# Optimization experiments

Measured on AMD Instinct MI355X. Metric: run time of the kernel, lower is better.

Reference implementation:

```python
import jax, jax.numpy as jnp
import numpy as np

NUM_EXPERTS = 8
TOP_K = 2
N_EMBD = 1024
D_FFN = 2048  # 4*N_EMBD // TOP_K, already multiple of BLOCK_N=128
BLOCK_M = 128
NORM_TOPK = True


def setup_inputs() -> dict:
    key = jax.random.key(0)
    k1, k2, k3 = jax.random.split(key, 3)
    x = jax.random.normal(k1, (2, 2048, N_EMBD), dtype=jnp.float32)
    router_w = jax.random.normal(k2, (NUM_EXPERTS, N_EMBD), dtype=jnp.float32) * 0.02
    w1 = jax.random.normal(k3, (N_EMBD, D_FFN * NUM_EXPERTS), dtype=jnp.float32) * 0.02
    return {"x": x, "router_w": router_w, "w1": w1}


def reference(x, router_w, w1):
    B, S, H = x.shape
    x_flat = x.reshape(-1, H)                                   # [T, H]
    router_logits = x_flat @ router_w.T                         # [T, E]
    probs = jax.nn.softmax(router_logits.astype(jnp.float32), axis=-1)
    rweights, sel = jax.lax.top_k(probs, TOP_K)                 # [T, k]
    if NORM_TOPK:
        rweights = rweights / rweights.sum(axis=-1, keepdims=True)
    rweights = rweights.astype(x.dtype)

    # repeat_interleave tokens top_k times, then stable-sort by expert id
    x_rep = jnp.repeat(x_flat, TOP_K, axis=0)                   # [M, H]
    sel_rep = sel.reshape(-1)                                   # [M]
    rw_rep = rweights.reshape(-1, 1)                            # [M, 1]
    order = jnp.argsort(sel_rep, stable=True)                   # expert-sort permutation
    x_grouped = x_rep[order]                                    # [M, H]
    sel_sorted = sel_rep[order]                                 # [M]
    rw_sorted = rw_rep[order]                                   # [M, 1]

    M = x_grouped.shape[0]
    nblk = M // BLOCK_M                                         # M divisible by BLOCK_M by construction
    # SDD kernel: expert of the first row of each BLOCK_M block selects w1 slice
    block_expert = sel_sorted[::BLOCK_M]                        # [nblk] == col_indices_ptr
    w1e = w1.reshape(H, NUM_EXPERTS, D_FFN)                     # w1[:, e*D:(e+1)*D] == w1e[:, e, :]
    w_blk = jnp.take(w1e, block_expert, axis=1)                 # [H, nblk, D]
    x_blk = x_grouped.reshape(nblk, BLOCK_M, H)                 # [nblk, Bm, H]
    block_sparse = jnp.einsum('bmh,hbd->bmd', x_blk, w_blk).reshape(M, D_FFN)

    block_sparse = jax.nn.gelu(block_sparse, approximate=False) * rw_sorted
    return block_sparse, router_logits
```

## Files before the change

### kernel.cpp

```cpp
#include <hip/hip_runtime.h>
#include <hip/hip_bf16.h>
#include <cmath>

typedef float f32x16 __attribute__((ext_vector_type(16)));
typedef __bf16 bf16x8 __attribute__((ext_vector_type(8)));
typedef __bf16 bf16x4 __attribute__((ext_vector_type(4)));

#define NE 8
#define H 1024
#define DF 2048
#define WCOLS 16384
#define NTOK 4096
#define MROWS 8192
#define NBLK 64


typedef const __attribute__((address_space(1))) unsigned int glb_u32;
typedef __attribute__((address_space(3))) unsigned int lds_u32;

__device__ __forceinline__ void async_load16(const void* g, void* l) {
    __builtin_amdgcn_global_load_lds((glb_u32*)g, (lds_u32*)l, 16, 0, 0);
}

__global__ __launch_bounds__(256) void prep_kernel(
    const float* __restrict__ x, const float* __restrict__ rw,
    const float* __restrict__ w1,
    float* __restrict__ logits, int* __restrict__ sel, float* __restrict__ rwn,
    __bf16* __restrict__ xb, __bf16* __restrict__ Wt)
{
    __shared__ float tile[32][132];
    int b = blockIdx.x;
    int tid = threadIdx.x;
    if (b < 1024) {
        int tok  = b * 4 + (tid >> 6);
        int lane = tid & 63;
        const float* xr = x + (size_t)tok * H;
        __bf16* xbr = xb + (size_t)tok * H;
        float acc[NE];
#pragma unroll
        for (int e = 0; e < NE; ++e) acc[e] = 0.f;
#pragma unroll
        for (int it = 0; it < 4; ++it) {
            int k = (it * 64 + lane) * 4;
            float4 xv = *(const float4*)(xr + k);
            bf16x4 xc;
            xc[0] = (__bf16)xv.x; xc[1] = (__bf16)xv.y;
            xc[2] = (__bf16)xv.z; xc[3] = (__bf16)xv.w;
            *(bf16x4*)(xbr + k) = xc;
#pragma unroll
            for (int e = 0; e < NE; ++e) {
                float4 wv = *(const float4*)(rw + e * H + k);
                acc[e] += xv.x * wv.x + xv.y * wv.y + xv.z * wv.z + xv.w * wv.w;
            }
        }
#pragma unroll
        for (int e = 0; e < NE; ++e) {
            float v = acc[e];
#pragma unroll
            for (int off = 32; off > 0; off >>= 1) v += __shfl_xor(v, off, 64);
            acc[e] = v;
        }
        if (lane == 0) {
#pragma unroll
            for (int e = 0; e < NE; ++e) logits[tok * NE + e] = acc[e];
            int i1 = 0; float m1 = acc[0];
#pragma unroll
            for (int e = 1; e < NE; ++e) if (acc[e] > m1) { m1 = acc[e]; i1 = e; }
            int i2 = -1; float m2 = -INFINITY;
#pragma unroll
            for (int e = 0; e < NE; ++e) if (e != i1 && acc[e] > m2) { m2 = acc[e]; i2 = e; }
            float e2 = expf(m2 - m1);
            float inv = 1.f / (1.f + e2);
            sel[tok * 2]     = i1;  sel[tok * 2 + 1] = i2;
            rwn[tok * 2]     = inv; rwn[tok * 2 + 1] = e2 * inv;
        }
        return;
    }
    int g  = b - 1024;
    int c  = g >> 5;
    int kb = g & 31;
    int kk = tid >> 3;
    int cc = (tid & 7) * 16;
    const float* src = w1 + (size_t)(kb * 32 + kk) * WCOLS + c * 128 + cc;
#pragma unroll
    for (int i = 0; i < 4; ++i) {
        float4 v = *(const float4*)(src + i * 4);
        *(float4*)&tile[kk][cc + i * 4] = v;
    }
    __syncthreads();
    int n = tid >> 1, kc0 = (tid & 1) * 16;
    bf16x8 o0, o1;
#pragma unroll
    for (int i = 0; i < 8; ++i) {
        o0[i] = (__bf16)tile[kc0 + i][n];
        o1[i] = (__bf16)tile[kc0 + 8 + i][n];
    }
    size_t tile_id = (size_t)(c >> 1) * 32 + kb;
    int group  = (c & 1) * 4 + (n >> 5);
    int chunk0 = kc0 >> 3;
    __bf16* dst = Wt + tile_id * 8192 + group * 1024 + chunk0 * 256 + (n & 31) * 8;
    *(bf16x8*)dst         = o0;
    *(bf16x8*)(dst + 256) = o1;
}

__global__ __launch_bounds__(256) void sort_kernel(
    const int* __restrict__ sel, const float* __restrict__ rwn,
    int* __restrict__ stok, float* __restrict__ srw, int* __restrict__ bexp)
{
    __shared__ int cnt[NE][256];
    __shared__ int wtot[NE];
    __shared__ int ebase[NE + 1];
    int t = threadIdx.x;
    int selv[32];
    int lc[NE];
#pragma unroll
    for (int e = 0; e < NE; ++e) lc[e] = 0;
    int base = t * 32;
#pragma unroll
    for (int j = 0; j < 32; ++j) { selv[j] = sel[base + j]; lc[selv[j]]++; }
#pragma unroll
    for (int e = 0; e < NE; ++e) cnt[e][t] = lc[e];
    __syncthreads();
    int l = t & 63;
#pragma unroll
    for (int ee = 0; ee < 2; ++ee) {
        int e = (t >> 6) * 2 + ee;
        int s = 0, pre[4];
#pragma unroll
        for (int i = 0; i < 4; ++i) { pre[i] = s; s += cnt[e][l * 4 + i]; }
        int inc = s;
#pragma unroll
        for (int d = 1; d < 64; d <<= 1) {
            int v = __shfl_up(inc, d, 64);
            if (l >= d) inc += v;
        }
        if (l == 63) wtot[e] = inc;
        int excl = inc - s;
#pragma unroll
        for (int i = 0; i < 4; ++i) cnt[e][l * 4 + i] = excl + pre[i];
    }
    __syncthreads();
    if (t == 0) {
        int acc = 0;
        for (int e = 0; e < NE; ++e) { ebase[e] = acc; acc += wtot[e]; }
        ebase[NE] = acc;
    }
    __syncthreads();
    int off[NE];
#pragma unroll
    for (int e = 0; e < NE; ++e) off[e] = ebase[e] + cnt[e][t];
#pragma unroll
    for (int j = 0; j < 32; ++j) {
        int i = base + j;
        int e = selv[j];
        int pos = off[e]++;
        stok[pos] = i >> 1;
        srw[pos]  = rwn[i];
    }
    __syncthreads();
    if (t < NBLK) {
        int r = t * 128;
        int e = 0;
        while (e < NE - 1 && r >= ebase[e + 1]) ++e;
        bexp[t] = e;
    }
}

__global__ __launch_bounds__(256, 4) void moe_gemm(
    const __bf16* __restrict__ xb, const __bf16* __restrict__ Wt,
    const int* __restrict__ stok, const float* __restrict__ srw,
    const int* __restrict__ bexp, float* __restrict__ out)
{
    __shared__ __align__(16) __bf16 smem[2 * 8192];
    __shared__ int   tokS[128];
    __shared__ float rwS[128];

    int g = blockIdx.x;
    int by = (g & 7) * 8 + ((g >> 3) & 7);
    int bx = g >> 6;
    int tid = threadIdx.x;
    if (tid < 128) {
        tokS[tid] = stok[by * 128 + tid];
        rwS[tid]  = srw[by * 128 + tid];
    }
    int e = bexp[by];
    __syncthreads();

    int lane = tid & 63;
    int wv   = tid >> 6;
    int l32  = lane & 31;
    int hi   = lane >> 5;

    int g0 = tid >> 7, c0_ = (tid >> 5) & 3, r0_ = tid & 31;
    int g1 = (tid + 256) >> 7, c1_ = ((tid + 256) >> 5) & 3;
    const __bf16* aSrc0 = xb + (size_t)tokS[g0 * 32 + r0_] * H + c0_ * 8;
    const __bf16* aSrc1 = xb + (size_t)tokS[g1 * 32 + r0_] * H + c1_ * 8;
    const __bf16* bSrcT = Wt + (size_t)(e * 8 + (bx >> 1)) * 262144
                             + (bx & 1) * 4096 + tid * 8;
    __bf16* aDstT = smem + tid * 8;
    __bf16* bDstT = smem + 4096 + tid * 8;

#define STAGE(kt_, bb_) do {                                                   \
        __bf16* ad_ = aDstT + (bb_) * 8192;                                    \
        async_load16(aSrc0 + (kt_) * 32, ad_);                                 \
        async_load16(aSrc1 + (kt_) * 32, ad_ + 2048);                          \
        const __bf16* b_ = bSrcT + (size_t)(kt_) * 8192;                       \
        __bf16* bd_ = bDstT + (bb_) * 8192;                                    \
        async_load16(b_,        bd_);                                          \
        async_load16(b_ + 2048, bd_ + 2048);                                   \
    } while (0)

    int wm  = (wv & 1) * 64;
    int wn  = (wv >> 1) * 64;
    int agb = (wv & 1) * 2;
    int bgb = (wv >> 1) * 2;
    int rdo = hi * 256 + l32 * 8;

    f32x16 acc[2][2];
#pragma unroll
    for (int i = 0; i < 2; ++i)
#pragma unroll
        for (int j = 0; j < 2; ++j)
#pragma unroll
            for (int r = 0; r < 16; ++r) acc[i][j][r] = 0.f;

    STAGE(0, 0);

    for (int kt = 0; kt < 32; ++kt) {
        int cur = kt & 1;
        __syncthreads();
        if (kt < 31) STAGE(kt + 1, 1 - cur);

        const __bf16* Ab = smem + cur * 8192;
        bf16x8 af[2][2], bfr[2][2];
#pragma unroll
        for (int h = 0; h < 2; ++h) {
            int co = h * 512 + rdo;
#pragma unroll
            for (int ti = 0; ti < 2; ++ti)
                af[ti][h]  = *(const bf16x8*)&Ab[(agb + ti) * 1024 + co];
#pragma unroll
            for (int tj = 0; tj < 2; ++tj)
                bfr[tj][h] = *(const bf16x8*)&Ab[4096 + (bgb + tj) * 1024 + co];
        }
#pragma unroll
        for (int h = 0; h < 2; ++h)
#pragma unroll
            for (int ti = 0; ti < 2; ++ti)
#pragma unroll
                for (int tj = 0; tj < 2; ++tj)
                    acc[ti][tj] = __builtin_amdgcn_mfma_f32_32x32x16_bf16(
                        af[ti][h], bfr[tj][h], acc[ti][tj], 0, 0, 0);
    }
#undef STAGE

    int rowh = hi * 4;
#pragma unroll
    for (int ti = 0; ti < 2; ++ti)
#pragma unroll
        for (int reg = 0; reg < 16; ++reg) {
            int row = (reg & 3) + 8 * (reg >> 2) + rowh;
            int m = wm + ti * 32 + row;
            float rw = rwS[m];
            size_t ob = (size_t)(by * 128 + m) * DF + bx * 128 + wn + l32;
#pragma unroll
            for (int tj = 0; tj < 2; ++tj) {
                float val = acc[ti][tj][reg];
                float u = 0.7978845608028654f * val * (1.f + 0.044715f * val * val);
                float t = __expf(-2.f * fabsf(u));
                float th = (1.f - t) / (1.f + t);
                th = u < 0.f ? -th : th;
                out[ob + tj * 32] = 0.5f * val * (1.f + th) * rw;
            }
        }
}

extern "C" void kernel_launch(void* const* d_in, const int* in_sizes, int n_in,
                              void* d_out, int out_size, void* d_ws, size_t ws_size,
                              hipStream_t stream) {
    (void)in_sizes; (void)n_in; (void)out_size; (void)ws_size;
    const float* x        = (const float*)d_in[0];
    const float* router_w = (const float*)d_in[1];
    const float* w1       = (const float*)d_in[2];
    float* out    = (float*)d_out;
    float* logits = out + (size_t)MROWS * DF;

    char* ws    = (char*)d_ws;
    int*   sel  = (int*)(ws);
    float* rwn  = (float*)(ws + 0x8000);
    int*   stok = (int*)(ws + 0x10000);
    float* srw  = (float*)(ws + 0x18000);
    int*   bexp = (int*)(ws + 0x20000);
    __bf16* xb  = (__bf16*)(ws + (1 << 20));
    __bf16* Wt  = (__bf16*)(ws + (1 << 20) + (8 << 20));

    prep_kernel<<<5120, 256, 0, stream>>>(x, router_w, w1, logits, sel, rwn, xb, Wt);
    sort_kernel<<<1, 256, 0, stream>>>(sel, rwn, stok, srw, bexp);
    moe_gemm<<<1024, 256, 0, stream>>>(xb, Wt, stok, srw, bexp, out);
}
```

Before: 196.1 us.

## Rewrite MoE GEMM as single-wave 64x64 tiles with register-prefetched B

The GEMM kernel moves from 256-thread blocks computing 128x128 tiles to 64-thread single-wave blocks computing 64x64 tiles, launched as 4096 blocks. B fragments are loaded straight from global into registers with double buffering, A is staged asynchronously into a small LDS double buffer with explicit vmcnt waits, and MFMA issue is raised with setprio. This removes block-wide barriers and shrinks LDS use to raise occupancy and overlap. In exchange each tile reuses data less, so global and L2 traffic rises, and global-to-register B loads may add latency.

```diff
diff --git a/kernel.cpp b/kernel.cpp
--- a/kernel.cpp
+++ b/kernel.cpp
@@ -166,113 +166,109 @@
     }
 }
 
-__global__ __launch_bounds__(256, 4) void moe_gemm(
+__global__ __launch_bounds__(64) void moe_gemm(
     const __bf16* __restrict__ xb, const __bf16* __restrict__ Wt,
     const int* __restrict__ stok, const float* __restrict__ srw,
     const int* __restrict__ bexp, float* __restrict__ out)
 {
-    __shared__ __align__(16) __bf16 smem[2 * 8192];
-    __shared__ int   tokS[128];
-    __shared__ float rwS[128];
-
-    int g = blockIdx.x;
-    int by = (g & 7) * 8 + ((g >> 3) & 7);
-    int bx = g >> 6;
-    int tid = threadIdx.x;
-    if (tid < 128) {
-        tokS[tid] = stok[by * 128 + tid];
-        rwS[tid]  = srw[by * 128 + tid];
-    }
-    int e = bexp[by];
-    __syncthreads();
-
-    int lane = tid & 63;
-    int wv   = tid >> 6;
+    __shared__ __align__(16) __bf16 smem[2 * 2048];
+
+    int g  = blockIdx.x;
+    int by = (g & 7) * 16 + ((g >> 3) & 15);
+    int bx = g >> 7;
+    int lane = threadIdx.x;
     int l32  = lane & 31;
     int hi   = lane >> 5;
-
-    int g0 = tid >> 7, c0_ = (tid >> 5) & 3, r0_ = tid & 31;
-    int g1 = (tid + 256) >> 7, c1_ = ((tid + 256) >> 5) & 3;
-    const __bf16* aSrc0 = xb + (size_t)tokS[g0 * 32 + r0_] * H + c0_ * 8;
-    const __bf16* aSrc1 = xb + (size_t)tokS[g1 * 32 + r0_] * H + c1_ * 8;
-    const __bf16* bSrcT = Wt + (size_t)(e * 8 + (bx >> 1)) * 262144
-                             + (bx & 1) * 4096 + tid * 8;
-    __bf16* aDstT = smem + tid * 8;
-    __bf16* bDstT = smem + 4096 + tid * 8;
-
-#define STAGE(kt_, bb_) do {                                                   \
-        __bf16* ad_ = aDstT + (bb_) * 8192;                                    \
-        async_load16(aSrc0 + (kt_) * 32, ad_);                                 \
-        async_load16(aSrc1 + (kt_) * 32, ad_ + 2048);                          \
-        const __bf16* b_ = bSrcT + (size_t)(kt_) * 8192;                       \
-        __bf16* bd_ = bDstT + (bb_) * 8192;                                    \
-        async_load16(b_,        bd_);                                          \
-        async_load16(b_ + 2048, bd_ + 2048);                                   \
-    } while (0)
-
-    int wm  = (wv & 1) * 64;
-    int wn  = (wv >> 1) * 64;
-    int agb = (wv & 1) * 2;
-    int bgb = (wv >> 1) * 2;
-    int rdo = hi * 256 + l32 * 8;
-
-    f32x16 acc[2][2];
-#pragma unroll
-    for (int i = 0; i < 2; ++i)
-#pragma unroll
-        for (int j = 0; j < 2; ++j)
-#pragma unroll
-            for (int r = 0; r < 16; ++r) acc[i][j][r] = 0.f;
-
-    STAGE(0, 0);
-
-    for (int kt = 0; kt < 32; ++kt) {
-        int cur = kt & 1;
-        __syncthreads();
-        if (kt < 31) STAGE(kt + 1, 1 - cur);
-
-        const __bf16* Ab = smem + cur * 8192;
-        bf16x8 af[2][2], bfr[2][2];
-#pragma unroll
-        for (int h = 0; h < 2; ++h) {
-            int co = h * 512 + rdo;
-#pragma unroll
-            for (int ti = 0; ti < 2; ++ti)
-                af[ti][h]  = *(const bf16x8*)&Ab[(agb + ti) * 1024 + co];
-#pragma unroll
-            for (int tj = 0; tj < 2; ++tj)
-                bfr[tj][h] = *(const bf16x8*)&Ab[4096 + (bgb + tj) * 1024 + co];
-        }
-#pragma unroll
-        for (int h = 0; h < 2; ++h)
-#pragma unroll
-            for (int ti = 0; ti < 2; ++ti)
-#pragma unroll
-                for (int tj = 0; tj < 2; ++tj)
-                    acc[ti][tj] = __builtin_amdgcn_mfma_f32_32x32x16_bf16(
-                        af[ti][h], bfr[tj][h], acc[ti][tj], 0, 0, 0);
-    }
-#undef STAGE
-
-    int rowh = hi * 4;
-#pragma unroll
-    for (int ti = 0; ti < 2; ++ti)
-#pragma unroll
-        for (int reg = 0; reg < 16; ++reg) {
-            int row = (reg & 3) + 8 * (reg >> 2) + rowh;
-            int m = wm + ti * 32 + row;
-            float rw = rwS[m];
-            size_t ob = (size_t)(by * 128 + m) * DF + bx * 128 + wn + l32;
-#pragma unroll
-            for (int tj = 0; tj < 2; ++tj) {
-                float val = acc[ti][tj][reg];
-                float u = 0.7978845608028654f * val * (1.f + 0.044715f * val * val);
-                float t = __expf(-2.f * fabsf(u));
-                float th = (1.f - t) / (1.f + t);
-                th = u < 0.f ? -th : th;
-                out[ob + tj * 32] = 0.5f * val * (1.f + th) * rw;
-            }
-        }
+    int rdo  = hi * 256 + l32 * 8;
+
+    int e    = bexp[by >> 1];
+    int tok0 = stok[by * 64 + l32];
+    int tok1 = stok[by * 64 + 32 + l32];
+    const __bf16* aS0 = xb + (size_t)tok0 * H + hi * 8;
+    const __bf16* aS1 = xb + (size_t)tok1 * H + hi * 8;
+    const __bf16* bB  = Wt + (size_t)(e * 8 + (bx >> 2)) * 262144
+                           + (size_t)((bx & 3) * 2) * 1024 + rdo;
+    __bf16* aD = smem + lane * 8;
+
+    f32x16 acc00, acc01, acc10, acc11;
+#pragma unroll
+    for (int r = 0; r < 16; ++r) { acc00[r] = 0.f; acc01[r] = 0.f;
+                                   acc10[r] = 0.f; acc11[r] = 0.f; }
+
+    bf16x8 bE[2][2], bO[2][2];
+
+    bE[0][0] = *(const bf16x8*)(bB);
+    bE[0][1] = *(const bf16x8*)(bB + 512);
+    bE[1][0] = *(const bf16x8*)(bB + 1024);
+    bE[1][1] = *(const bf16x8*)(bB + 1536);
+    __builtin_amdgcn_sched_barrier(0);
+    async_load16(aS0,      aD);          async_load16(aS0 + 16, aD + 512);
+    async_load16(aS1,      aD + 1024);   async_load16(aS1 + 16, aD + 1536);
+    async_load16(aS0 + 32, aD + 2048);   async_load16(aS0 + 48, aD + 2560);
+    async_load16(aS1 + 32, aD + 3072);   async_load16(aS1 + 48, aD + 3584);
+
+#define ITER(t_, bC_, bN_, DOB_, DOA_, VN_) do {                               \
+    asm volatile("s_waitcnt vmcnt(" #VN_ ")" ::: "memory");                    \
+    __builtin_amdgcn_sched_barrier(0);                                         \
+    const __bf16* Ab_ = smem + ((t_) & 1) * 2048;                              \
+    bf16x8 af00 = *(const bf16x8*)(Ab_ + rdo);                                 \
+    bf16x8 af01 = *(const bf16x8*)(Ab_ + rdo + 512);                           \
+    bf16x8 af10 = *(const bf16x8*)(Ab_ + rdo + 1024);                          \
+    bf16x8 af11 = *(const bf16x8*)(Ab_ + rdo + 1536);                          \
+    asm volatile("s_waitcnt lgkmcnt(0)" ::: "memory");                         \
+    __builtin_amdgcn_sched_barrier(0);                                         \
+    if (DOB_) {                                                                \
+        const __bf16* bp_ = bB + (size_t)((t_) + 1) * 8192;                    \
+        bN_[0][0] = *(const bf16x8*)(bp_);                                     \
+        bN_[0][1] = *(const bf16x8*)(bp_ + 512);                               \
+        bN_[1][0] = *(const bf16x8*)(bp_ + 1024);                              \
+        bN_[1][1] = *(const bf16x8*)(bp_ + 1536);                              \
+    }                                                                          \
+    __builtin_amdgcn_sched_barrier(0);                                         \
+    if (DOA_) {                                                                \
+        const __bf16* a0_ = aS0 + ((t_) + 2) * 32;                             \
+        const __bf16* a1_ = aS1 + ((t_) + 2) * 32;                             \
+        __bf16* ad_ = aD + ((t_) & 1) * 2048;                                  \
+        async_load16(a0_,      ad_);        async_load16(a0_ + 16, ad_ + 512); \
+        async_load16(a1_,      ad_ + 1024); async_load16(a1_ + 16, ad_ + 1536);\
+    }                                                                          \
+    __builtin_amdgcn_s_setprio(1);                                             \
+    acc00 = __builtin_amdgcn_mfma_f32_32x32x16_bf16(af00, bC_[0][0], acc00, 0, 0, 0); \
+    acc01 = __builtin_amdgcn_mfma_f32_32x32x16_bf16(af00, bC_[1][0], acc01, 0, 0, 0); \
+    acc10 = __builtin_amdgcn_mfma_f32_32x32x16_bf16(af10, bC_[0][0], acc10, 0, 0, 0); \
+    acc11 = __builtin_amdgcn_mfma_f32_32x32x16_bf16(af10, bC_[1][0], acc11, 0, 0, 0); \
+    acc00 = __builtin_amdgcn_mfma_f32_32x32x16_bf16(af01, bC_[0][1], acc00, 0, 0, 0); \
+    acc01 = __builtin_amdgcn_mfma_f32_32x32x16_bf16(af01, bC_[1][1], acc01, 0, 0, 0); \
+    acc10 = __builtin_amdgcn_mfma_f32_32x32x16_bf16(af11, bC_[0][1], acc10, 0, 0, 0); \
+    acc11 = __builtin_amdgcn_mfma_f32_32x32x16_bf16(af11, bC_[1][1], acc11, 0, 0, 0); \
+    __builtin_amdgcn_s_setprio(0);                                             \
+} while (0)
+
+    for (int kt = 0; kt < 30; kt += 2) {
+        ITER(kt,     bE, bO, 1, 1, 4);
+        ITER(kt + 1, bO, bE, 1, 1, 4);
+    }
+    ITER(30, bE, bO, 1, 0, 4);
+    ITER(31, bO, bE, 0, 0, 0);
+#undef ITER
+
+    const float* rwp = srw + by * 64;
+    float* outp = out + (size_t)(by * 64) * DF + (size_t)bx * 64 + l32;
+#define EPI(ACC_, ti_, tj_) _Pragma("unroll")                                  \
+    for (int reg = 0; reg < 16; ++reg) {                                       \
+        int row = (reg & 3) + 8 * (reg >> 2) + 4 * hi + (ti_) * 32;            \
+        float val = ACC_[reg];                                                 \
+        float u = 0.7978845608028654f * val * (1.f + 0.044715f * val * val);   \
+        float t = __expf(-2.f * fabsf(u));                                     \
+        float th = (1.f - t) / (1.f + t);                                      \
+        th = u < 0.f ? -th : th;                                               \
+        outp[(size_t)row * DF + (tj_) * 32] = 0.5f * val * (1.f + th) * rwp[row]; \
+    }
+    EPI(acc00, 0, 0)
+    EPI(acc01, 0, 1)
+    EPI(acc10, 1, 0)
+    EPI(acc11, 1, 1)
+#undef EPI
 }
 
 extern "C" void kernel_launch(void* const* d_in, const int* in_sizes, int n_in,
@@ -296,5 +292,5 @@
 
     prep_kernel<<<5120, 256, 0, stream>>>(x, router_w, w1, logits, sel, rwn, xb, Wt);
     sort_kernel<<<1, 256, 0, stream>>>(sel, rwn, stok, srw, bexp);
-    moe_gemm<<<1024, 256, 0, stream>>>(xb, Wt, stok, srw, bexp, out);
-}
+    moe_gemm<<<4096, 64, 0, stream>>>(xb, Wt, stok, srw, bexp, out);
+}
```

Measured after the change: 230.5 us. +17.6%, slower.

## Overlap single-block sort with weight conversion; use nontemporal loads and stores

Applied to the files above, without the earlier changes.

Splits the prep kernel into a router kernel and a mid kernel. The mid kernel runs the w1 transpose/bf16 conversion blocks alongside the single-block sort, so the serial sort no longer has its own launch and can hide behind the bandwidth-bound conversion. It also switches the w1 loads and the GEMM output stores to nontemporal hints to reduce cache pollution. The risks are that the sort block may be scheduled last and sit on the critical path, and that scalarized nontemporal loads may vectorize less well.

```diff
diff --git a/kernel.cpp b/kernel.cpp
--- a/kernel.cpp
+++ b/kernel.cpp
@@ -22,95 +22,101 @@
     __builtin_amdgcn_global_load_lds((glb_u32*)g, (lds_u32*)l, 16, 0, 0);
 }
 
-__global__ __launch_bounds__(256) void prep_kernel(
+__global__ __launch_bounds__(256) void router_kernel(
     const float* __restrict__ x, const float* __restrict__ rw,
-    const float* __restrict__ w1,
     float* __restrict__ logits, int* __restrict__ sel, float* __restrict__ rwn,
-    __bf16* __restrict__ xb, __bf16* __restrict__ Wt)
+    __bf16* __restrict__ xb)
 {
-    __shared__ float tile[32][132];
     int b = blockIdx.x;
     int tid = threadIdx.x;
-    if (b < 1024) {
-        int tok  = b * 4 + (tid >> 6);
-        int lane = tid & 63;
-        const float* xr = x + (size_t)tok * H;
-        __bf16* xbr = xb + (size_t)tok * H;
-        float acc[NE];
-#pragma unroll
-        for (int e = 0; e < NE; ++e) acc[e] = 0.f;
-#pragma unroll
-        for (int it = 0; it < 4; ++it) {
-            int k = (it * 64 + lane) * 4;
-            float4 xv = *(const float4*)(xr + k);
-            bf16x4 xc;
-            xc[0] = (__bf16)xv.x; xc[1] = (__bf16)xv.y;
-            xc[2] = (__bf16)xv.z; xc[3] = (__bf16)xv.w;
-            *(bf16x4*)(xbr + k) = xc;
-#pragma unroll
-            for (int e = 0; e < NE; ++e) {
-                float4 wv = *(const float4*)(rw + e * H + k);
-                acc[e] += xv.x * wv.x + xv.y * wv.y + xv.z * wv.z + xv.w * wv.w;
-            }
-        }
+    int tok  = b * 4 + (tid >> 6);
+    int lane = tid & 63;
+    const float* xr = x + (size_t)tok * H;
+    __bf16* xbr = xb + (size_t)tok * H;
+    float acc[NE];
+#pragma unroll
+    for (int e = 0; e < NE; ++e) acc[e] = 0.f;
+#pragma unroll
+    for (int it = 0; it < 4; ++it) {
+        int k = (it * 64 + lane) * 4;
+        float4 xv = *(const float4*)(xr + k);
+        bf16x4 xc;
+        xc[0] = (__bf16)xv.x; xc[1] = (__bf16)xv.y;
+        xc[2] = (__bf16)xv.z; xc[3] = (__bf16)xv.w;
+        *(bf16x4*)(xbr + k) = xc;
 #pragma unroll
         for (int e = 0; e < NE; ++e) {
-            float v = acc[e];
-#pragma unroll
-            for (int off = 32; off > 0; off >>= 1) v += __shfl_xor(v, off, 64);
-            acc[e] = v;
-        }
-        if (lane == 0) {
-#pragma unroll
-            for (int e = 0; e < NE; ++e) logits[tok * NE + e] = acc[e];
-            int i1 = 0; float m1 = acc[0];
-#pragma unroll
-            for (int e = 1; e < NE; ++e) if (acc[e] > m1) { m1 = acc[e]; i1 = e; }
-            int i2 = -1; float m2 = -INFINITY;
-#pragma unroll
-            for (int e = 0; e < NE; ++e) if (e != i1 && acc[e] > m2) { m2 = acc[e]; i2 = e; }
-            float e2 = expf(m2 - m1);
-            float inv = 1.f / (1.f + e2);
-            sel[tok * 2]     = i1;  sel[tok * 2 + 1] = i2;
-            rwn[tok * 2]     = inv; rwn[tok * 2 + 1] = e2 * inv;
-        }
-        return;
-    }
-    int g  = b - 1024;
-    int c  = g >> 5;
-    int kb = g & 31;
-    int kk = tid >> 3;
-    int cc = (tid & 7) * 16;
-    const float* src = w1 + (size_t)(kb * 32 + kk) * WCOLS + c * 128 + cc;
-#pragma unroll
-    for (int i = 0; i < 4; ++i) {
-        float4 v = *(const float4*)(src + i * 4);
-        *(float4*)&tile[kk][cc + i * 4] = v;
-    }
-    __syncthreads();
-    int n = tid >> 1, kc0 = (tid & 1) * 16;
-    bf16x8 o0, o1;
-#pragma unroll
-    for (int i = 0; i < 8; ++i) {
-        o0[i] = (__bf16)tile[kc0 + i][n];
-        o1[i] = (__bf16)tile[kc0 + 8 + i][n];
-    }
-    size_t tile_id = (size_t)(c >> 1) * 32 + kb;
-    int group  = (c & 1) * 4 + (n >> 5);
-    int chunk0 = kc0 >> 3;
-    __bf16* dst = Wt + tile_id * 8192 + group * 1024 + chunk0 * 256 + (n & 31) * 8;
-    *(bf16x8*)dst         = o0;
-    *(bf16x8*)(dst + 256) = o1;
-}
-
-__global__ __launch_bounds__(256) void sort_kernel(
+            float4 wv = *(const float4*)(rw + e * H + k);
+            acc[e] += xv.x * wv.x + xv.y * wv.y + xv.z * wv.z + xv.w * wv.w;
+        }
+    }
+#pragma unroll
+    for (int e = 0; e < NE; ++e) {
+        float v = acc[e];
+#pragma unroll
+        for (int off = 32; off > 0; off >>= 1) v += __shfl_xor(v, off, 64);
+        acc[e] = v;
+    }
+    if (lane == 0) {
+#pragma unroll
+        for (int e = 0; e < NE; ++e) logits[tok * NE + e] = acc[e];
+        int i1 = 0; float m1 = acc[0];
+#pragma unroll
+        for (int e = 1; e < NE; ++e) if (acc[e] > m1) { m1 = acc[e]; i1 = e; }
+        int i2 = -1; float m2 = -INFINITY;
+#pragma unroll
+        for (int e = 0; e < NE; ++e) if (e != i1 && acc[e] > m2) { m2 = acc[e]; i2 = e; }
+        float e2 = expf(m2 - m1);
+        float inv = 1.f / (1.f + e2);
+        sel[tok * 2]     = i1;  sel[tok * 2 + 1] = i2;
+        rwn[tok * 2]     = inv; rwn[tok * 2 + 1] = e2 * inv;
+    }
+}
+
+__global__ __launch_bounds__(256) void mid_kernel(
+    const float* __restrict__ w1, __bf16* __restrict__ Wt,
     const int* __restrict__ sel, const float* __restrict__ rwn,
     int* __restrict__ stok, float* __restrict__ srw, int* __restrict__ bexp)
 {
+    __shared__ float tile[32][132];
     __shared__ int cnt[NE][256];
     __shared__ int wtot[NE];
     __shared__ int ebase[NE + 1];
+    int b = blockIdx.x;
     int t = threadIdx.x;
+
+    if (b < 4096) {
+        int c  = b >> 5;
+        int kb = b & 31;
+        int kk = t >> 3;
+        int cc = (t & 7) * 16;
+        const float* src = w1 + (size_t)(kb * 32 + kk) * WCOLS + c * 128 + cc;
+#pragma unroll
+        for (int i = 0; i < 4; ++i) {
+            float4 v;
+            v.x = __builtin_nontemporal_load(src + i * 4);
+            v.y = __builtin_nontemporal_load(src + i * 4 + 1);
+            v.z = __builtin_nontemporal_load(src + i * 4 + 2);
+            v.w = __builtin_nontemporal_load(src + i * 4 + 3);
+            *(float4*)&tile[kk][cc + i * 4] = v;
+        }
+        __syncthreads();
+        int n = t >> 1, kc0 = (t & 1) * 16;
+        bf16x8 o0, o1;
+#pragma unroll
+        for (int i = 0; i < 8; ++i) {
+            o0[i] = (__bf16)tile[kc0 + i][n];
+            o1[i] = (__bf16)tile[kc0 + 8 + i][n];
+        }
+        size_t tile_id = (size_t)(c >> 1) * 32 + kb;
+        int group  = (c & 1) * 4 + (n >> 5);
+        int chunk0 = kc0 >> 3;
+        __bf16* dst = Wt + tile_id * 8192 + group * 1024 + chunk0 * 256 + (n & 31) * 8;
+        *(bf16x8*)dst         = o0;
+        *(bf16x8*)(dst + 256) = o1;
+        return;
+    }
+
     int selv[32];
     int lc[NE];
 #pragma unroll
@@ -270,7 +276,8 @@
                 float t = __expf(-2.f * fabsf(u));
                 float th = (1.f - t) / (1.f + t);
                 th = u < 0.f ? -th : th;
-                out[ob + tj * 32] = 0.5f * val * (1.f + th) * rw;
+                __builtin_nontemporal_store(0.5f * val * (1.f + th) * rw,
+                                            &out[ob + tj * 32]);
             }
         }
 }
@@ -294,7 +301,7 @@
     __bf16* xb  = (__bf16*)(ws + (1 << 20));
     __bf16* Wt  = (__bf16*)(ws + (1 << 20) + (8 << 20));
 
-    prep_kernel<<<5120, 256, 0, stream>>>(x, router_w, w1, logits, sel, rwn, xb, Wt);
-    sort_kernel<<<1, 256, 0, stream>>>(sel, rwn, stok, srw, bexp);
+    router_kernel<<<1024, 256, 0, stream>>>(x, router_w, logits, sel, rwn, xb);
+    mid_kernel<<<4097, 256, 0, stream>>>(w1, Wt, sel, rwn, stok, srw, bexp);
     moe_gemm<<<1024, 256, 0, stream>>>(xb, Wt, stok, srw, bexp, out);
 }
```

Measured after the change: 195.0 us. No clear change (-0.5%).
